# Kernel optimization log

Hardware: AMD Instinct MI355X
Metric: run time of the kernel (lower is better)

## Reference

```python
import jax, jax.numpy as jnp
import numpy as np

L2_NORM_CLIP = 1.0
NOISE_MUL = 0.1


def setup_inputs() -> dict:
    key = jax.random.key(0)
    ks = jax.random.split(key, 6)
    B, S, D, K = 8, 4096, 1024, 1024
    scale = 1.0 / np.sqrt(D)
    return {
        "q": jax.random.normal(ks[0], (B, 1, D), dtype=jnp.float32),
        "k": jax.random.normal(ks[1], (B, S, D), dtype=jnp.float32),
        "v": jax.random.normal(ks[2], (B, S, D), dtype=jnp.float32),
        "wq_w": jax.random.normal(ks[3], (D, K), dtype=jnp.float32) * scale,
        "wq_b": jnp.zeros((K,), dtype=jnp.float32),
        "wk_w": jax.random.normal(ks[4], (D, K), dtype=jnp.float32) * scale,
        "wk_b": jnp.zeros((K,), dtype=jnp.float32),
        "wv_w": jax.random.normal(ks[5], (D, K), dtype=jnp.float32) * scale,
        "wv_b": jnp.zeros((K,), dtype=jnp.float32),
    }


def reference(q, k, v, wq_w, wq_b, wk_w, wk_b, wv_w, wv_b):
    # Dense projections: [B,1,K], [B,S,K], [B,S,K]
    fq = q @ wq_w + wq_b
    fk = k @ wk_w + wk_b
    fv = v @ wv_w + wv_b

    # Sigmoid attention: [B,1,S]
    dk = jnp.asarray(fk.shape[-1], dtype=fq.dtype)
    logits = jnp.einsum("bqk,bsk->bqs", fq, fk) / jnp.sqrt(dk)
    attention_weights = jax.nn.sigmoid(logits)

    # Per-token L2 clip of values over feature axis
    v_norm = jnp.linalg.norm(fv, ord=2, axis=2, keepdims=True) / L2_NORM_CLIP
    fv_clipped = fv / jnp.maximum(1.0, v_norm)

    # Weight values and reduce over sequence: [B,1,K]
    fv_w = fv_clipped * jnp.transpose(attention_weights, (0, 2, 1))  # [B,S,K]
    seed = jnp.sum(fv_w, axis=1, keepdims=True)

    # Gaussian noise injection (fixed key for determinism)
    noise_key = jax.random.key(1234)
    noise = jax.random.normal(noise_key, seed.shape, dtype=seed.dtype)
    seed = seed + noise * (NOISE_MUL * L2_NORM_CLIP)
    return (seed, attention_weights)
```

## Files before the change

### kernel.cpp

```cpp
#include <hip/hip_runtime.h>
#include <stdint.h>


#define Bn 8
#define Sn 4096
#define Dn 1024
#define Kn 1024

typedef unsigned short u16;
typedef __attribute__((ext_vector_type(4))) unsigned short u16x4;
typedef __attribute__((ext_vector_type(8))) unsigned short u16x8;
typedef __attribute__((ext_vector_type(8))) __bf16 bf16x8;
typedef __attribute__((ext_vector_type(4))) float f32x4;

__device__ __forceinline__ u16 f2bf(float f) {
  uint32_t x = __float_as_uint(f);
  x += 0x7FFFu + ((x >> 16) & 1u);
  return (u16)(x >> 16);
}
__device__ __forceinline__ float bf2f(u16 h) {
  return __uint_as_float(((uint32_t)h) << 16);
}

__device__ __forceinline__ uint32_t rotl32(uint32_t x, int d) {
  return (x << d) | (x >> (32 - d));
}
__device__ void threefry2x32(uint32_t k0, uint32_t k1, uint32_t x0, uint32_t x1,
                             uint32_t* o0, uint32_t* o1) {
  uint32_t ks0 = k0, ks1 = k1, ks2 = k0 ^ k1 ^ 0x1BD11BDAu;
  x0 += ks0; x1 += ks1;
#define TF_R4(a,b,c,d) \
  x0 += x1; x1 = rotl32(x1,a); x1 ^= x0; \
  x0 += x1; x1 = rotl32(x1,b); x1 ^= x0; \
  x0 += x1; x1 = rotl32(x1,c); x1 ^= x0; \
  x0 += x1; x1 = rotl32(x1,d); x1 ^= x0;
  TF_R4(13,15,26,6);  x0 += ks1; x1 += ks2 + 1u;
  TF_R4(17,29,16,24); x0 += ks2; x1 += ks0 + 2u;
  TF_R4(13,15,26,6);  x0 += ks0; x1 += ks1 + 3u;
  TF_R4(17,29,16,24); x0 += ks1; x1 += ks2 + 4u;
  TF_R4(13,15,26,6);  x0 += ks2; x1 += ks0 + 5u;
#undef TF_R4
  *o0 = x0; *o1 = x1;
}

__device__ float erfinv_f(float x) {
  float w = -log1pf(-x * x);
  float p;
  if (w < 5.0f) {
    w -= 2.5f;
    p = 2.81022636e-08f;
    p = fmaf(p, w, 3.43273939e-07f);
    p = fmaf(p, w, -3.5233877e-06f);
    p = fmaf(p, w, -4.39150654e-06f);
    p = fmaf(p, w, 0.00021858087f);
    p = fmaf(p, w, -0.00125372503f);
    p = fmaf(p, w, -0.00417768164f);
    p = fmaf(p, w, 0.246640727f);
    p = fmaf(p, w, 1.50140941f);
  } else {
    w = sqrtf(w) - 3.0f;
    p = -0.000200214257f;
    p = fmaf(p, w, 0.000100950558f);
    p = fmaf(p, w, 0.00134934322f);
    p = fmaf(p, w, -0.00367342844f);
    p = fmaf(p, w, 0.00573950773f);
    p = fmaf(p, w, -0.0076224613f);
    p = fmaf(p, w, 0.00943887047f);
    p = fmaf(p, w, 1.00167406f);
    p = fmaf(p, w, 2.83297682f);
  }
  return p * x;
}

__global__ void k_fq(const float* __restrict__ q, const float* __restrict__ wq,
                     const float* __restrict__ bq, float* __restrict__ fq) {
  int blk = blockIdx.x;
  int b = blk >> 5, jc = (blk >> 3) & 3, dc = blk & 7;
  int j = jc * 256 + threadIdx.x;
  const float* qb = q + b * Dn;
  float acc = 0.f;
  int d0 = dc * 128;
  for (int d = d0; d < d0 + 128; ++d)
    acc = fmaf(qb[d], wq[(size_t)d * Kn + j], acc);
  if (dc == 0) acc += bq[j];
  atomicAdd(&fq[b * Kn + j], acc);
}

__global__ void k_g(const float* __restrict__ wk, const float* __restrict__ fq,
                    float* __restrict__ g) {
  int wid = (blockIdx.x * 256 + threadIdx.x) >> 6;
  int lane = threadIdx.x & 63;
  int b = wid >> 10, d = wid & 1023;
  const float* row = wk + (size_t)d * Kn;
  const float* f = fq + b * Kn;
  float acc = 0.f;
  for (int j = lane; j < Kn; j += 64) acc = fmaf(row[j], f[j], acc);
  for (int m = 32; m; m >>= 1) acc += __shfl_xor(acc, m, 64);
  if (lane == 0) g[b * Dn + d] = acc;
}

__global__ void k_cb(const float* __restrict__ fq, const float* __restrict__ bk,
                     float* __restrict__ cb) {
  int b = threadIdx.x >> 6;
  int lane = threadIdx.x & 63;
  float acc = 0.f;
  for (int j = lane; j < Kn; j += 64) acc = fmaf(fq[b * Kn + j], bk[j], acc);
  for (int m = 32; m; m >>= 1) acc += __shfl_xor(acc, m, 64);
  if (lane == 0) cb[b] = acc;
}

__global__ void k_twv(const float* __restrict__ wv, u16* __restrict__ wvt) {
  __shared__ u16 tile[64][72];
  int k0 = (blockIdx.x & 15) * 64, n0 = (blockIdx.x >> 4) * 64;
  int tid = threadIdx.x;
  int r = tid >> 2, c0 = (tid & 3) * 16;
#pragma unroll
  for (int i = 0; i < 4; ++i) {
    float4 vv = *reinterpret_cast<const float4*>(wv + (size_t)(k0 + r) * Kn + n0 + c0 + i * 4);
    tile[r][c0 + i * 4 + 0] = f2bf(vv.x);
    tile[r][c0 + i * 4 + 1] = f2bf(vv.y);
    tile[r][c0 + i * 4 + 2] = f2bf(vv.z);
    tile[r][c0 + i * 4 + 3] = f2bf(vv.w);
  }
  __syncthreads();
  int n = tid >> 2, kc = (tid & 3) * 16;
  alignas(16) u16 o[16];
#pragma unroll
  for (int i = 0; i < 16; ++i) o[i] = tile[kc + i][n];
  *reinterpret_cast<u16x8*>(wvt + (size_t)(n0 + n) * Kn + k0 + kc)     = *reinterpret_cast<u16x8*>(&o[0]);
  *reinterpret_cast<u16x8*>(wvt + (size_t)(n0 + n) * Kn + k0 + kc + 8) = *reinterpret_cast<u16x8*>(&o[8]);
}

__global__ void k_tv(const float* __restrict__ v, u16* __restrict__ vb) {
  size_t t = (size_t)blockIdx.x * 256 + threadIdx.x;
  const float4* p = reinterpret_cast<const float4*>(v + t * 8);
  float4 a = p[0], b = p[1];
  u16x8 o = { f2bf(a.x), f2bf(a.y), f2bf(a.z), f2bf(a.w),
              f2bf(b.x), f2bf(b.y), f2bf(b.z), f2bf(b.w) };
  *reinterpret_cast<u16x8*>(vb + t * 8) = o;
}

__global__ void k_attn(const float* __restrict__ kmat, const float* __restrict__ g,
                       const float* __restrict__ cb, float* __restrict__ out_attn,
                       float* __restrict__ attn_ws) {
  int row = blockIdx.x * 4 + (threadIdx.x >> 6);
  int lane = threadIdx.x & 63;
  int b = row >> 12;
  const float4* kr = reinterpret_cast<const float4*>(kmat + (size_t)row * Dn);
  const float4* gr = reinterpret_cast<const float4*>(g + b * Dn);
  float acc = 0.f;
#pragma unroll
  for (int i = 0; i < 4; ++i) {
    float4 kv = kr[lane + 64 * i];
    float4 gv = gr[lane + 64 * i];
    acc = fmaf(kv.x, gv.x, acc); acc = fmaf(kv.y, gv.y, acc);
    acc = fmaf(kv.z, gv.z, acc); acc = fmaf(kv.w, gv.w, acc);
  }
  for (int m = 32; m; m >>= 1) acc += __shfl_xor(acc, m, 64);
  if (lane == 0) {
    float logit = (acc + cb[b]) * 0.03125f;
    float s = 1.f / (1.f + expf(-logit));
    out_attn[row] = s;
    attn_ws[row] = s;
  }
}

__global__ __launch_bounds__(256)
void k_norm2(const u16* __restrict__ vb, const u16* __restrict__ wvt,
             const float* __restrict__ bv, float* __restrict__ norm2) {
  int blk = blockIdx.x;
  int b  = blk >> 8;
  int nb = (blk >> 5) & 7;
  int sb = blk & 31;
  int s0 = sb * 128, n0 = nb * 128;

  __shared__ u16 As[128 * 64];
  __shared__ u16 Bs[128 * 64];
  __shared__ float nrm[128];

  int tid = threadIdx.x;
  int wave = tid >> 6, lane = tid & 63;
  int wr = wave & 1, wc = wave >> 1;
  int m = lane & 15, q = lane >> 4;

  f32x4 acc[4][4];
#pragma unroll
  for (int i = 0; i < 4; ++i)
#pragma unroll
    for (int j = 0; j < 4; ++j) acc[i][j] = (f32x4){0.f, 0.f, 0.f, 0.f};
  if (tid < 128) nrm[tid] = 0.f;

  int lrow = lane >> 3;
  int lchunk = (lane & 7) ^ lrow;
  const u16* gA0 = vb  + ((size_t)(b * Sn + s0) + lrow) * 1024 + lchunk * 8;
  const u16* gB0 = wvt + ((size_t)(n0 + lrow)) * 1024 + lchunk * 8;

  for (int k0 = 0; k0 < 1024; k0 += 64) {
    __syncthreads();
#pragma unroll
    for (int t = 0; t < 4; ++t) {
      int u = wave * 4 + t;
      __builtin_amdgcn_global_load_lds(
          (const __attribute__((address_space(1))) void*)(gA0 + (size_t)u * 8 * 1024 + k0),
          (__attribute__((address_space(3))) void*)(&As[u * 512]), 16, 0, 0);
      __builtin_amdgcn_global_load_lds(
          (const __attribute__((address_space(1))) void*)(gB0 + (size_t)u * 8 * 1024 + k0),
          (__attribute__((address_space(3))) void*)(&Bs[u * 512]), 16, 0, 0);
    }
    __syncthreads();

    bf16x8 a[4][2], bf[4][2];
#pragma unroll
    for (int rt = 0; rt < 4; ++rt) {
      int r = wr * 64 + rt * 16 + m;
#pragma unroll
      for (int j = 0; j < 2; ++j) {
        int c = j * 4 + q;
        u16x8 raw = *reinterpret_cast<const u16x8*>(&As[r * 64 + ((c ^ (r & 7)) * 8)]);
        a[rt][j] = __builtin_bit_cast(bf16x8, raw);
      }
    }
#pragma unroll
    for (int ct = 0; ct < 4; ++ct) {
      int n = wc * 64 + ct * 16 + m;
#pragma unroll
      for (int j = 0; j < 2; ++j) {
        int c = j * 4 + q;
        u16x8 raw = *reinterpret_cast<const u16x8*>(&Bs[n * 64 + ((c ^ (n & 7)) * 8)]);
        bf[ct][j] = __builtin_bit_cast(bf16x8, raw);
      }
    }
#pragma unroll
    for (int j = 0; j < 2; ++j)
#pragma unroll
      for (int rt = 0; rt < 4; ++rt)
#pragma unroll
        for (int ct = 0; ct < 4; ++ct)
          acc[rt][ct] = __builtin_amdgcn_mfma_f32_16x16x32_bf16(a[rt][j], bf[ct][j],
                                                                acc[rt][ct], 0, 0, 0);
  }

  float bvv[4];
#pragma unroll
  for (int ct = 0; ct < 4; ++ct) bvv[ct] = bv[n0 + wc * 64 + ct * 16 + m];

#pragma unroll
  for (int rt = 0; rt < 4; ++rt) {
#pragma unroll
    for (int reg = 0; reg < 4; ++reg) {
      float ss = 0.f;
#pragma unroll
      for (int ct = 0; ct < 4; ++ct) {
        float f = acc[rt][ct][reg] + bvv[ct];
        ss = fmaf(f, f, ss);
      }
      ss += __shfl_xor(ss, 1, 64);
      ss += __shfl_xor(ss, 2, 64);
      ss += __shfl_xor(ss, 4, 64);
      ss += __shfl_xor(ss, 8, 64);
      if (m == 0) {
        int r = wr * 64 + rt * 16 + q * 4 + reg;
        atomicAdd(&nrm[r], ss);
      }
    }
  }
  __syncthreads();
  if (tid < 128) atomicAdd(&norm2[b * Sn + s0 + tid], nrm[tid]);
}

__global__ void k_wsum(const u16* __restrict__ vb, const float* __restrict__ attn,
                       const float* __restrict__ norm2, float* __restrict__ y,
                       float* __restrict__ csum) {
  int blk = blockIdx.x;
  int b = blk >> 6;
  int sc = (blk & 63) * 64;
  __shared__ float coef[64];
  int tid = threadIdx.x;
  if (tid < 64) {
    int s = sc + tid;
    coef[tid] = attn[b * Sn + s] / fmaxf(1.f, sqrtf(norm2[b * Sn + s]));
  }
  __syncthreads();
  if (tid == 0) {
    float cs = 0.f;
    for (int i = 0; i < 64; ++i) cs += coef[i];
    atomicAdd(&csum[b], cs);
  }
  const u16* vbb = vb + ((size_t)b * Sn + sc) * Dn;
  int d0 = tid * 4;
  float a0 = 0.f, a1 = 0.f, a2 = 0.f, a3 = 0.f;
  for (int i = 0; i < 64; ++i) {
    float c = coef[i];
    u16x4 r = *reinterpret_cast<const u16x4*>(vbb + (size_t)i * Dn + d0);
    a0 = fmaf(c, bf2f(r[0]), a0); a1 = fmaf(c, bf2f(r[1]), a1);
    a2 = fmaf(c, bf2f(r[2]), a2); a3 = fmaf(c, bf2f(r[3]), a3);
  }
  atomicAdd(&y[b * Dn + d0 + 0], a0);
  atomicAdd(&y[b * Dn + d0 + 1], a1);
  atomicAdd(&y[b * Dn + d0 + 2], a2);
  atomicAdd(&y[b * Dn + d0 + 3], a3);
}

__global__ void k_seed(const float* __restrict__ y, const float* __restrict__ wv,
                       const float* __restrict__ bv, const float* __restrict__ csum,
                       float* __restrict__ out_seed) {
  int blk = blockIdx.x;
  int b = blk >> 5, jc = (blk >> 3) & 3, dc = blk & 7;
  int j = jc * 256 + threadIdx.x;
  const float* yb = y + b * Dn;
  float acc = 0.f;
  int d0 = dc * 128;
  for (int d = d0; d < d0 + 128; ++d)
    acc = fmaf(yb[d], wv[(size_t)d * Kn + j], acc);
  if (dc == 0) {
    acc += csum[b] * bv[j];
    int t = b * Kn + j;
    uint32_t o0, o1;
    threefry2x32(0u, 1234u, 0u, (uint32_t)t, &o0, &o1);
    uint32_t bits = o0 ^ o1;
    float f = __uint_as_float((bits >> 9) | 0x3F800000u) - 1.0f;
    float lo = __uint_as_float(0xBF7FFFFFu);
    float u = f * (1.0f - lo) + lo;
    u = fmaxf(u, lo);
    acc += 1.41421356237f * erfinv_f(u) * 0.1f;
  }
  atomicAdd(&out_seed[b * Kn + j], acc);
}

extern "C" void kernel_launch(void* const* d_in, const int* in_sizes, int n_in,
                              void* d_out, int out_size, void* d_ws, size_t ws_size,
                              hipStream_t stream) {
  const float* q  = (const float*)d_in[0];
  const float* k  = (const float*)d_in[1];
  const float* v  = (const float*)d_in[2];
  const float* wq = (const float*)d_in[3];
  const float* bq = (const float*)d_in[4];
  const float* wk = (const float*)d_in[5];
  const float* bk = (const float*)d_in[6];
  const float* wv = (const float*)d_in[7];
  const float* bv = (const float*)d_in[8];
  float* out = (float*)d_out;
  float* ws = (float*)d_ws;

  float* fq      = ws;
  float* g       = ws + 8192;
  float* cb      = ws + 16384;
  float* csum    = ws + 16392;
  float* norm2   = ws + 16896;
  float* y       = ws + 49664;
  float* attn_ws = ws + 57856;
  u16* wvt = (u16*)((char*)d_ws + 393216);
  u16* vb  = (u16*)((char*)d_ws + (4 << 20));

  hipMemsetAsync(ws, 0, 57856 * sizeof(float), stream);
  hipMemsetAsync(out, 0, 8192 * sizeof(float), stream);
  k_fq  <<<256,   256, 0, stream>>>(q, wq, bq, fq);
  k_g   <<<2048,  256, 0, stream>>>(wk, fq, g);
  k_cb  <<<1,     512, 0, stream>>>(fq, bk, cb);
  k_twv <<<256,   256, 0, stream>>>(wv, wvt);
  k_attn<<<8192,  256, 0, stream>>>(k, g, cb, out + 8192, attn_ws);
  for (int h = 0; h < 2; ++h) {
    const float* vh = v + (size_t)h * 4 * Sn * Dn;
    k_tv   <<<8192, 256, 0, stream>>>(vh, vb);
    k_norm2<<<1024, 256, 0, stream>>>(vb, wvt, bv, norm2 + (size_t)h * 4 * Sn);
    k_wsum <<<256,  256, 0, stream>>>(vb, attn_ws + (size_t)h * 4 * Sn,
                                      norm2 + (size_t)h * 4 * Sn,
                                      y + (size_t)h * 4 * Dn, csum + h * 4);
  }
  k_seed<<<256,   256, 0, stream>>>(y, wv, bv, csum, out);
}
```

Measured before the change: 446.3 us.

## Fuse V conversion, projection, norm and weighted sum into one MFMA kernel

Replaces the separate bf16 conversion of V, the norm GEMM, the weighted-sum pass and the final seed GEMV with a single kernel. It loads fp32 V directly with register prefetch, computes the full 1024-wide projected row block per workgroup, derives per-row clip coefficients and reduces the coefficient-weighted projected values straight into the seed accumulator. This avoids writing and re-reading the bf16 V copy and the separate Wv GEMV, and the small prep kernels are merged to cut launches. In exchange, B operands are read from global memory instead of LDS, only 512 workgroups run, and register pressure rises with 32 accumulator tiles per wave.

```diff
diff --git a/kernel.cpp b/kernel.cpp
--- a/kernel.cpp
+++ b/kernel.cpp
@@ -8,7 +8,6 @@
 #define Kn 1024
 
 typedef unsigned short u16;
-typedef __attribute__((ext_vector_type(4))) unsigned short u16x4;
 typedef __attribute__((ext_vector_type(8))) unsigned short u16x8;
 typedef __attribute__((ext_vector_type(8))) __bf16 bf16x8;
 typedef __attribute__((ext_vector_type(4))) float f32x4;
@@ -17,9 +16,6 @@
   uint32_t x = __float_as_uint(f);
   x += 0x7FFFu + ((x >> 16) & 1u);
   return (u16)(x >> 16);
-}
-__device__ __forceinline__ float bf2f(u16 h) {
-  return __uint_as_float(((uint32_t)h) << 16);
 }
 
 __device__ __forceinline__ uint32_t rotl32(uint32_t x, int d) {
@@ -72,72 +68,65 @@
   return p * x;
 }
 
-__global__ void k_fq(const float* __restrict__ q, const float* __restrict__ wq,
-                     const float* __restrict__ bq, float* __restrict__ fq) {
-  int blk = blockIdx.x;
-  int b = blk >> 5, jc = (blk >> 3) & 3, dc = blk & 7;
-  int j = jc * 256 + threadIdx.x;
-  const float* qb = q + b * Dn;
-  float acc = 0.f;
-  int d0 = dc * 128;
-  for (int d = d0; d < d0 + 128; ++d)
-    acc = fmaf(qb[d], wq[(size_t)d * Kn + j], acc);
-  if (dc == 0) acc += bq[j];
-  atomicAdd(&fq[b * Kn + j], acc);
-}
-
-__global__ void k_g(const float* __restrict__ wk, const float* __restrict__ fq,
-                    float* __restrict__ g) {
-  int wid = (blockIdx.x * 256 + threadIdx.x) >> 6;
-  int lane = threadIdx.x & 63;
-  int b = wid >> 10, d = wid & 1023;
-  const float* row = wk + (size_t)d * Kn;
-  const float* f = fq + b * Kn;
-  float acc = 0.f;
-  for (int j = lane; j < Kn; j += 64) acc = fmaf(row[j], f[j], acc);
-  for (int m = 32; m; m >>= 1) acc += __shfl_xor(acc, m, 64);
-  if (lane == 0) g[b * Dn + d] = acc;
-}
-
-__global__ void k_cb(const float* __restrict__ fq, const float* __restrict__ bk,
-                     float* __restrict__ cb) {
-  int b = threadIdx.x >> 6;
-  int lane = threadIdx.x & 63;
-  float acc = 0.f;
-  for (int j = lane; j < Kn; j += 64) acc = fmaf(fq[b * Kn + j], bk[j], acc);
-  for (int m = 32; m; m >>= 1) acc += __shfl_xor(acc, m, 64);
-  if (lane == 0) cb[b] = acc;
-}
-
-__global__ void k_twv(const float* __restrict__ wv, u16* __restrict__ wvt) {
+__global__ void k_prep(const float* __restrict__ q, const float* __restrict__ wq,
+                       const float* __restrict__ bq, float* __restrict__ fq,
+                       const float* __restrict__ wv, u16* __restrict__ wvt) {
   __shared__ u16 tile[64][72];
-  int k0 = (blockIdx.x & 15) * 64, n0 = (blockIdx.x >> 4) * 64;
   int tid = threadIdx.x;
-  int r = tid >> 2, c0 = (tid & 3) * 16;
-#pragma unroll
-  for (int i = 0; i < 4; ++i) {
-    float4 vv = *reinterpret_cast<const float4*>(wv + (size_t)(k0 + r) * Kn + n0 + c0 + i * 4);
-    tile[r][c0 + i * 4 + 0] = f2bf(vv.x);
-    tile[r][c0 + i * 4 + 1] = f2bf(vv.y);
-    tile[r][c0 + i * 4 + 2] = f2bf(vv.z);
-    tile[r][c0 + i * 4 + 3] = f2bf(vv.w);
-  }
-  __syncthreads();
-  int n = tid >> 2, kc = (tid & 3) * 16;
-  alignas(16) u16 o[16];
-#pragma unroll
-  for (int i = 0; i < 16; ++i) o[i] = tile[kc + i][n];
-  *reinterpret_cast<u16x8*>(wvt + (size_t)(n0 + n) * Kn + k0 + kc)     = *reinterpret_cast<u16x8*>(&o[0]);
-  *reinterpret_cast<u16x8*>(wvt + (size_t)(n0 + n) * Kn + k0 + kc + 8) = *reinterpret_cast<u16x8*>(&o[8]);
-}
-
-__global__ void k_tv(const float* __restrict__ v, u16* __restrict__ vb) {
-  size_t t = (size_t)blockIdx.x * 256 + threadIdx.x;
-  const float4* p = reinterpret_cast<const float4*>(v + t * 8);
-  float4 a = p[0], b = p[1];
-  u16x8 o = { f2bf(a.x), f2bf(a.y), f2bf(a.z), f2bf(a.w),
-              f2bf(b.x), f2bf(b.y), f2bf(b.z), f2bf(b.w) };
-  *reinterpret_cast<u16x8*>(vb + t * 8) = o;
+  if (blockIdx.x < 256) {
+    int blk = blockIdx.x;
+    int b = blk >> 5, jc = (blk >> 3) & 3, dc = blk & 7;
+    int j = jc * 256 + tid;
+    const float* qb = q + b * Dn;
+    float acc = 0.f;
+    int d0 = dc * 128;
+    for (int d = d0; d < d0 + 128; ++d)
+      acc = fmaf(qb[d], wq[(size_t)d * Kn + j], acc);
+    if (dc == 0) acc += bq[j];
+    atomicAdd(&fq[b * Kn + j], acc);
+  } else {
+    int idx = blockIdx.x - 256;
+    int k0 = (idx & 15) * 64, n0 = (idx >> 4) * 64;
+    int r = tid >> 2, c0 = (tid & 3) * 16;
+#pragma unroll
+    for (int i = 0; i < 4; ++i) {
+      float4 vv = *reinterpret_cast<const float4*>(wv + (size_t)(k0 + r) * Kn + n0 + c0 + i * 4);
+      tile[r][c0 + i * 4 + 0] = f2bf(vv.x);
+      tile[r][c0 + i * 4 + 1] = f2bf(vv.y);
+      tile[r][c0 + i * 4 + 2] = f2bf(vv.z);
+      tile[r][c0 + i * 4 + 3] = f2bf(vv.w);
+    }
+    __syncthreads();
+    int n = tid >> 2, kc = (tid & 3) * 16;
+    alignas(16) u16 o[16];
+#pragma unroll
+    for (int i = 0; i < 16; ++i) o[i] = tile[kc + i][n];
+    *reinterpret_cast<u16x8*>(wvt + (size_t)(n0 + n) * Kn + k0 + kc)     = *reinterpret_cast<u16x8*>(&o[0]);
+    *reinterpret_cast<u16x8*>(wvt + (size_t)(n0 + n) * Kn + k0 + kc + 8) = *reinterpret_cast<u16x8*>(&o[8]);
+  }
+}
+
+__global__ void k_gcb(const float* __restrict__ wk, const float* __restrict__ fq,
+                      const float* __restrict__ bk, float* __restrict__ g,
+                      float* __restrict__ cb) {
+  int tid = threadIdx.x;
+  if (blockIdx.x < 2048) {
+    int wid = (blockIdx.x * 256 + tid) >> 6;
+    int lane = tid & 63;
+    int b = wid >> 10, d = wid & 1023;
+    const float* row = wk + (size_t)d * Kn;
+    const float* f = fq + b * Kn;
+    float acc = 0.f;
+    for (int j = lane; j < Kn; j += 64) acc = fmaf(row[j], f[j], acc);
+    for (int m = 32; m; m >>= 1) acc += __shfl_xor(acc, m, 64);
+    if (lane == 0) g[b * Dn + d] = acc;
+  } else if (tid < 64) {
+    int b = blockIdx.x - 2048;
+    float acc = 0.f;
+    for (int j = tid; j < Kn; j += 64) acc = fmaf(fq[b * Kn + j], bk[j], acc);
+    for (int m = 32; m; m >>= 1) acc += __shfl_xor(acc, m, 64);
+    if (tid == 0) cb[b] = acc;
+  }
 }
 
 __global__ void k_attn(const float* __restrict__ kmat, const float* __restrict__ g,
@@ -165,84 +154,76 @@
   }
 }
 
-__global__ __launch_bounds__(256)
-void k_norm2(const u16* __restrict__ vb, const u16* __restrict__ wvt,
-             const float* __restrict__ bv, float* __restrict__ norm2) {
-  int blk = blockIdx.x;
-  int b  = blk >> 8;
-  int nb = (blk >> 5) & 7;
-  int sb = blk & 31;
-  int s0 = sb * 128, n0 = nb * 128;
-
-  __shared__ u16 As[128 * 64];
-  __shared__ u16 Bs[128 * 64];
-  __shared__ float nrm[128];
+__global__ __launch_bounds__(512, 2)
+void k_fv(const float* __restrict__ v, const u16* __restrict__ wvt,
+          const float* __restrict__ bv, const float* __restrict__ attn,
+          float* __restrict__ seed_acc) {
+  __shared__ u16 As[64 * 64];
+  __shared__ float nrm[64];
+  __shared__ float coef[64];
+
+  int r0 = blockIdx.x * 64;
+  int b  = r0 >> 12;
+  int s0 = r0 & (Sn - 1);
 
   int tid = threadIdx.x;
   int wave = tid >> 6, lane = tid & 63;
-  int wr = wave & 1, wc = wave >> 1;
-  int m = lane & 15, q = lane >> 4;
-
-  f32x4 acc[4][4];
+  int m = lane & 15, qq = lane >> 4;
+
+  if (tid < 64) nrm[tid] = 0.f;
+
+  f32x4 acc[4][8];
 #pragma unroll
   for (int i = 0; i < 4; ++i)
 #pragma unroll
-    for (int j = 0; j < 4; ++j) acc[i][j] = (f32x4){0.f, 0.f, 0.f, 0.f};
-  if (tid < 128) nrm[tid] = 0.f;
-
-  int lrow = lane >> 3;
-  int lchunk = (lane & 7) ^ lrow;
-  const u16* gA0 = vb  + ((size_t)(b * Sn + s0) + lrow) * 1024 + lchunk * 8;
-  const u16* gB0 = wvt + ((size_t)(n0 + lrow)) * 1024 + lchunk * 8;
+    for (int j = 0; j < 8; ++j) acc[i][j] = (f32x4){0.f, 0.f, 0.f, 0.f};
+
+  int arow = tid >> 3, achunk = tid & 7;
+  const float* gA0 = v + ((size_t)(b * Sn + s0) + arow) * Dn + achunk * 8;
+  int apos = (achunk ^ (arow & 7)) * 8;
+
+  const u16* gB = wvt + (size_t)(wave * 128 + m) * Kn;
+
+  float4 pa0 = reinterpret_cast<const float4*>(gA0)[0];
+  float4 pa1 = reinterpret_cast<const float4*>(gA0)[1];
 
   for (int k0 = 0; k0 < 1024; k0 += 64) {
     __syncthreads();
-#pragma unroll
-    for (int t = 0; t < 4; ++t) {
-      int u = wave * 4 + t;
-      __builtin_amdgcn_global_load_lds(
-          (const __attribute__((address_space(1))) void*)(gA0 + (size_t)u * 8 * 1024 + k0),
-          (__attribute__((address_space(3))) void*)(&As[u * 512]), 16, 0, 0);
-      __builtin_amdgcn_global_load_lds(
-          (const __attribute__((address_space(1))) void*)(gB0 + (size_t)u * 8 * 1024 + k0),
-          (__attribute__((address_space(3))) void*)(&Bs[u * 512]), 16, 0, 0);
+    {
+      u16x8 o = { f2bf(pa0.x), f2bf(pa0.y), f2bf(pa0.z), f2bf(pa0.w),
+                  f2bf(pa1.x), f2bf(pa1.y), f2bf(pa1.z), f2bf(pa1.w) };
+      *reinterpret_cast<u16x8*>(&As[arow * 64 + apos]) = o;
+    }
+    if (k0 < 960) {
+      const float4* pa = reinterpret_cast<const float4*>(gA0 + k0 + 64);
+      pa0 = pa[0]; pa1 = pa[1];
     }
     __syncthreads();
 
-    bf16x8 a[4][2], bf[4][2];
-#pragma unroll
-    for (int rt = 0; rt < 4; ++rt) {
-      int r = wr * 64 + rt * 16 + m;
-#pragma unroll
-      for (int j = 0; j < 2; ++j) {
-        int c = j * 4 + q;
+#pragma unroll
+    for (int j = 0; j < 2; ++j) {
+      int c = j * 4 + qq;
+      bf16x8 a[4];
+#pragma unroll
+      for (int rt = 0; rt < 4; ++rt) {
+        int r = rt * 16 + m;
         u16x8 raw = *reinterpret_cast<const u16x8*>(&As[r * 64 + ((c ^ (r & 7)) * 8)]);
-        a[rt][j] = __builtin_bit_cast(bf16x8, raw);
+        a[rt] = __builtin_bit_cast(bf16x8, raw);
       }
-    }
-#pragma unroll
-    for (int ct = 0; ct < 4; ++ct) {
-      int n = wc * 64 + ct * 16 + m;
-#pragma unroll
-      for (int j = 0; j < 2; ++j) {
-        int c = j * 4 + q;
-        u16x8 raw = *reinterpret_cast<const u16x8*>(&Bs[n * 64 + ((c ^ (n & 7)) * 8)]);
-        bf[ct][j] = __builtin_bit_cast(bf16x8, raw);
+#pragma unroll
+      for (int ct = 0; ct < 8; ++ct) {
+        u16x8 raw = *reinterpret_cast<const u16x8*>(gB + (size_t)ct * 16 * Kn + k0 + c * 8);
+        bf16x8 bb = __builtin_bit_cast(bf16x8, raw);
+#pragma unroll
+        for (int rt = 0; rt < 4; ++rt)
+          acc[rt][ct] = __builtin_amdgcn_mfma_f32_16x16x32_bf16(a[rt], bb, acc[rt][ct], 0, 0, 0);
       }
     }
-#pragma unroll
-    for (int j = 0; j < 2; ++j)
-#pragma unroll
-      for (int rt = 0; rt < 4; ++rt)
-#pragma unroll
-        for (int ct = 0; ct < 4; ++ct)
-          acc[rt][ct] = __builtin_amdgcn_mfma_f32_16x16x32_bf16(a[rt][j], bf[ct][j],
-                                                                acc[rt][ct], 0, 0, 0);
-  }
-
-  float bvv[4];
-#pragma unroll
-  for (int ct = 0; ct < 4; ++ct) bvv[ct] = bv[n0 + wc * 64 + ct * 16 + m];
+  }
+
+  float bvv[8];
+#pragma unroll
+  for (int ct = 0; ct < 8; ++ct) bvv[ct] = bv[wave * 128 + ct * 16 + m];
 
 #pragma unroll
   for (int rt = 0; rt < 4; ++rt) {
@@ -250,7 +231,7 @@
     for (int reg = 0; reg < 4; ++reg) {
       float ss = 0.f;
 #pragma unroll
-      for (int ct = 0; ct < 4; ++ct) {
+      for (int ct = 0; ct < 8; ++ct) {
         float f = acc[rt][ct][reg] + bvv[ct];
         ss = fmaf(f, f, ss);
       }
@@ -258,73 +239,41 @@
       ss += __shfl_xor(ss, 2, 64);
       ss += __shfl_xor(ss, 4, 64);
       ss += __shfl_xor(ss, 8, 64);
-      if (m == 0) {
-        int r = wr * 64 + rt * 16 + q * 4 + reg;
-        atomicAdd(&nrm[r], ss);
+      if (m == 0) atomicAdd(&nrm[rt * 16 + qq * 4 + reg], ss);
+    }
+  }
+  __syncthreads();
+  if (tid < 64)
+    coef[tid] = attn[b * Sn + s0 + tid] / fmaxf(1.f, sqrtf(nrm[tid]));
+  __syncthreads();
+
+#pragma unroll
+  for (int ct = 0; ct < 8; ++ct) {
+    float t = 0.f;
+#pragma unroll
+    for (int rt = 0; rt < 4; ++rt) {
+#pragma unroll
+      for (int reg = 0; reg < 4; ++reg) {
+        float cf = coef[rt * 16 + qq * 4 + reg];
+        t = fmaf(cf, acc[rt][ct][reg] + bvv[ct], t);
       }
     }
-  }
-  __syncthreads();
-  if (tid < 128) atomicAdd(&norm2[b * Sn + s0 + tid], nrm[tid]);
-}
-
-__global__ void k_wsum(const u16* __restrict__ vb, const float* __restrict__ attn,
-                       const float* __restrict__ norm2, float* __restrict__ y,
-                       float* __restrict__ csum) {
-  int blk = blockIdx.x;
-  int b = blk >> 6;
-  int sc = (blk & 63) * 64;
-  __shared__ float coef[64];
-  int tid = threadIdx.x;
-  if (tid < 64) {
-    int s = sc + tid;
-    coef[tid] = attn[b * Sn + s] / fmaxf(1.f, sqrtf(norm2[b * Sn + s]));
-  }
-  __syncthreads();
-  if (tid == 0) {
-    float cs = 0.f;
-    for (int i = 0; i < 64; ++i) cs += coef[i];
-    atomicAdd(&csum[b], cs);
-  }
-  const u16* vbb = vb + ((size_t)b * Sn + sc) * Dn;
-  int d0 = tid * 4;
-  float a0 = 0.f, a1 = 0.f, a2 = 0.f, a3 = 0.f;
-  for (int i = 0; i < 64; ++i) {
-    float c = coef[i];
-    u16x4 r = *reinterpret_cast<const u16x4*>(vbb + (size_t)i * Dn + d0);
-    a0 = fmaf(c, bf2f(r[0]), a0); a1 = fmaf(c, bf2f(r[1]), a1);
-    a2 = fmaf(c, bf2f(r[2]), a2); a3 = fmaf(c, bf2f(r[3]), a3);
-  }
-  atomicAdd(&y[b * Dn + d0 + 0], a0);
-  atomicAdd(&y[b * Dn + d0 + 1], a1);
-  atomicAdd(&y[b * Dn + d0 + 2], a2);
-  atomicAdd(&y[b * Dn + d0 + 3], a3);
-}
-
-__global__ void k_seed(const float* __restrict__ y, const float* __restrict__ wv,
-                       const float* __restrict__ bv, const float* __restrict__ csum,
-                       float* __restrict__ out_seed) {
-  int blk = blockIdx.x;
-  int b = blk >> 5, jc = (blk >> 3) & 3, dc = blk & 7;
-  int j = jc * 256 + threadIdx.x;
-  const float* yb = y + b * Dn;
-  float acc = 0.f;
-  int d0 = dc * 128;
-  for (int d = d0; d < d0 + 128; ++d)
-    acc = fmaf(yb[d], wv[(size_t)d * Kn + j], acc);
-  if (dc == 0) {
-    acc += csum[b] * bv[j];
-    int t = b * Kn + j;
-    uint32_t o0, o1;
-    threefry2x32(0u, 1234u, 0u, (uint32_t)t, &o0, &o1);
-    uint32_t bits = o0 ^ o1;
-    float f = __uint_as_float((bits >> 9) | 0x3F800000u) - 1.0f;
-    float lo = __uint_as_float(0xBF7FFFFFu);
-    float u = f * (1.0f - lo) + lo;
-    u = fmaxf(u, lo);
-    acc += 1.41421356237f * erfinv_f(u) * 0.1f;
-  }
-  atomicAdd(&out_seed[b * Kn + j], acc);
+    t += __shfl_xor(t, 16, 64);
+    t += __shfl_xor(t, 32, 64);
+    if (qq == 0) atomicAdd(&seed_acc[b * Kn + wave * 128 + ct * 16 + m], t);
+  }
+}
+
+__global__ void k_final(const float* __restrict__ seed_acc, float* __restrict__ out) {
+  int t = blockIdx.x * 256 + threadIdx.x;
+  uint32_t o0, o1;
+  threefry2x32(0u, 1234u, 0u, (uint32_t)t, &o0, &o1);
+  uint32_t bits = o0 ^ o1;
+  float f = __uint_as_float((bits >> 9) | 0x3F800000u) - 1.0f;
+  float lo = __uint_as_float(0xBF7FFFFFu);
+  float u = f * (1.0f - lo) + lo;
+  u = fmaxf(u, lo);
+  out[t] = seed_acc[t] + 1.41421356237f * erfinv_f(u) * 0.1f;
 }
 
 extern "C" void kernel_launch(void* const* d_in, const int* in_sizes, int n_in,
@@ -342,30 +291,17 @@
   float* out = (float*)d_out;
   float* ws = (float*)d_ws;
 
-  float* fq      = ws;
-  float* g       = ws + 8192;
-  float* cb      = ws + 16384;
-  float* csum    = ws + 16392;
-  float* norm2   = ws + 16896;
-  float* y       = ws + 49664;
-  float* attn_ws = ws + 57856;
-  u16* wvt = (u16*)((char*)d_ws + 393216);
-  u16* vb  = (u16*)((char*)d_ws + (4 << 20));
-
-  hipMemsetAsync(ws, 0, 57856 * sizeof(float), stream);
-  hipMemsetAsync(out, 0, 8192 * sizeof(float), stream);
-  k_fq  <<<256,   256, 0, stream>>>(q, wq, bq, fq);
-  k_g   <<<2048,  256, 0, stream>>>(wk, fq, g);
-  k_cb  <<<1,     512, 0, stream>>>(fq, bk, cb);
-  k_twv <<<256,   256, 0, stream>>>(wv, wvt);
-  k_attn<<<8192,  256, 0, stream>>>(k, g, cb, out + 8192, attn_ws);
-  for (int h = 0; h < 2; ++h) {
-    const float* vh = v + (size_t)h * 4 * Sn * Dn;
-    k_tv   <<<8192, 256, 0, stream>>>(vh, vb);
-    k_norm2<<<1024, 256, 0, stream>>>(vb, wvt, bv, norm2 + (size_t)h * 4 * Sn);
-    k_wsum <<<256,  256, 0, stream>>>(vb, attn_ws + (size_t)h * 4 * Sn,
-                                      norm2 + (size_t)h * 4 * Sn,
-                                      y + (size_t)h * 4 * Dn, csum + h * 4);
-  }
-  k_seed<<<256,   256, 0, stream>>>(y, wv, bv, csum, out);
-}
+  float* fq       = ws;
+  float* seed_acc = ws + 8192;
+  float* g        = ws + 16384;
+  float* cb       = ws + 24576;
+  float* attn_ws  = ws + 24832;
+  u16* wvt = (u16*)((char*)d_ws + 262144);
+
+  hipMemsetAsync(ws, 0, 16384 * sizeof(float), stream);
+  k_prep <<<512,  256, 0, stream>>>(q, wq, bq, fq, wv, wvt);
+  k_gcb  <<<2056, 256, 0, stream>>>(wk, fq, bk, g, cb);
+  k_attn <<<8192, 256, 0, stream>>>(k, g, cb, out + 8192, attn_ws);
+  k_fv   <<<512,  512, 0, stream>>>(v, wvt, bv, attn_ws, seed_acc);
+  k_final<<<32,   256, 0, stream>>>(seed_acc, out);
+}
```

After: 433.5 us. -2.9%, faster.
